# Kernel optimization log

Measured on AMD Instinct MI355X. Metric: run time of the kernel, lower is better.

## Reference

```python
import jax, jax.numpy as jnp
import numpy as np


def setup_inputs() -> dict:
    key = jax.random.key(0)
    B, C, L = 8, 32, 131072
    x = jax.random.normal(key, (B, C, L), dtype=jnp.float32)
    return {"x": x, "kernel_size": 9}


def reference(x, kernel_size):
    # x: [B, C, L]; replicate-pad last dim by (k-1)//2 on each side,
    # take sliding windows of size k, return per-window median.
    k = kernel_size
    p = (k - 1) // 2
    L = x.shape[-1]
    xp = jnp.pad(x, ((0, 0), (0, 0), (p, p)), mode="edge")  # [B, C, L+k-1]
    # Stack k shifted views -> [k, B, C, L] (loop over small fixed k only)
    win = jnp.stack([xp[..., i:i + L] for i in range(k)], axis=0)
    # k is odd, so the exact middle of the sorted window is the median
    # (matches torch.median's lower-median convention for odd k).
    return jnp.sort(win, axis=0)[k // 2]
```

## Files before the change

kernel.cpp:

```cpp
#include <hip/hip_runtime.h>


typedef float f32x4 __attribute__((ext_vector_type(4)));

#define CE(a, b) do { float _mn = fminf(a, b); (b) = fmaxf(a, b); (a) = _mn; } while (0)

__device__ __forceinline__ float median9(float p0, float p1, float p2,
                                         float p3, float p4, float p5,
                                         float p6, float p7, float p8) {
    CE(p1, p2); CE(p4, p5); CE(p7, p8);
    CE(p0, p1); CE(p3, p4); CE(p6, p7);
    CE(p1, p2); CE(p4, p5); CE(p7, p8);
    CE(p0, p3); CE(p5, p8); CE(p4, p7);
    CE(p3, p6); CE(p1, p4); CE(p2, p5);
    CE(p4, p7); CE(p4, p2); CE(p6, p4);
    CE(p4, p2);
    return p4;
}

constexpr int kL         = 131072;
constexpr int kTotal     = 8 * 32 * kL;
constexpr int kPerThread = 8;

__global__ __launch_bounds__(256)
void med9_f32_kernel(const float* __restrict__ in, float* __restrict__ out) {
    int t    = blockIdx.x * 256 + threadIdx.x;
    int base = t * kPerThread;
    int col  = base & (kL - 1);
    const float* __restrict__ rin = in + (base - col);

    float v[16];
    if (col >= 4 && col + 12 <= kL) {
        f32x4 a = *reinterpret_cast<const f32x4*>(rin + col - 4);
        f32x4 b = *reinterpret_cast<const f32x4*>(rin + col);
        f32x4 c = *reinterpret_cast<const f32x4*>(rin + col + 4);
        f32x4 d = *reinterpret_cast<const f32x4*>(rin + col + 8);
        v[0]  = a.x; v[1]  = a.y; v[2]  = a.z; v[3]  = a.w;
        v[4]  = b.x; v[5]  = b.y; v[6]  = b.z; v[7]  = b.w;
        v[8]  = c.x; v[9]  = c.y; v[10] = c.z; v[11] = c.w;
        v[12] = d.x; v[13] = d.y; v[14] = d.z; v[15] = d.w;
    } else {
#pragma unroll
        for (int j = 0; j < 16; ++j) {
            int idx = col - 4 + j;
            idx = idx < 0 ? 0 : (idx > kL - 1 ? kL - 1 : idx);
            v[j] = rin[idx];
        }
    }

    f32x4 r0, r1;
    r0.x = median9(v[0], v[1], v[2],  v[3],  v[4],  v[5],  v[6],  v[7],  v[8]);
    r0.y = median9(v[1], v[2], v[3],  v[4],  v[5],  v[6],  v[7],  v[8],  v[9]);
    r0.z = median9(v[2], v[3], v[4],  v[5],  v[6],  v[7],  v[8],  v[9],  v[10]);
    r0.w = median9(v[3], v[4], v[5],  v[6],  v[7],  v[8],  v[9],  v[10], v[11]);
    r1.x = median9(v[4], v[5], v[6],  v[7],  v[8],  v[9],  v[10], v[11], v[12]);
    r1.y = median9(v[5], v[6], v[7],  v[8],  v[9],  v[10], v[11], v[12], v[13]);
    r1.z = median9(v[6], v[7], v[8],  v[9],  v[10], v[11], v[12], v[13], v[14]);
    r1.w = median9(v[7], v[8], v[9],  v[10], v[11], v[12], v[13], v[14], v[15]);

    __builtin_nontemporal_store(r0, reinterpret_cast<f32x4*>(out + base));
    __builtin_nontemporal_store(r1, reinterpret_cast<f32x4*>(out + base + 4));
}

extern "C" void kernel_launch(void* const* d_in, const int* in_sizes, int n_in,
                              void* d_out, int out_size, void* d_ws, size_t ws_size,
                              hipStream_t stream) {
    const float* x = (const float*)d_in[0];
    float* out = (float*)d_out;

    int nthreads = kTotal / kPerThread;
    int block = 256;
    int grid = nthreads / block;
    med9_f32_kernel<<<grid, block, 0, stream>>>(x, out);
}
```

Measured before the change: 54.43 us.

## Compute 9-point median via shared 3-element sorted triples and fmed3

Replaces the per-output 19-compare-exchange median network with the classic median-of-medians decomposition. Each consecutive triple of inputs is reduced once to min, med and max using min3/max3/fmed3, and every output's median is then taken from three overlapping triples. The triples are shared across the 8 outputs each thread produces, which cuts ALU work. Nontemporal stores are also replaced by regular stores. The kernel is likely memory-bound, so the reduced arithmetic may matter little.

```diff
diff --git a/kernel.cpp b/kernel.cpp
--- a/kernel.cpp
+++ b/kernel.cpp
@@ -3,29 +3,22 @@
 
 typedef float f32x4 __attribute__((ext_vector_type(4)));
 
-#define CE(a, b) do { float _mn = fminf(a, b); (b) = fmaxf(a, b); (a) = _mn; } while (0)
-
-__device__ __forceinline__ float median9(float p0, float p1, float p2,
-                                         float p3, float p4, float p5,
-                                         float p6, float p7, float p8) {
-    CE(p1, p2); CE(p4, p5); CE(p7, p8);
-    CE(p0, p1); CE(p3, p4); CE(p6, p7);
-    CE(p1, p2); CE(p4, p5); CE(p7, p8);
-    CE(p0, p3); CE(p5, p8); CE(p4, p7);
-    CE(p3, p6); CE(p1, p4); CE(p2, p5);
-    CE(p4, p7); CE(p4, p2); CE(p6, p4);
-    CE(p4, p2);
-    return p4;
+__device__ __forceinline__ float min3f(float a, float b, float c) {
+    return fminf(fminf(a, b), c);
+}
+__device__ __forceinline__ float max3f(float a, float b, float c) {
+    return fmaxf(fmaxf(a, b), c);
+}
+__device__ __forceinline__ float med3f(float a, float b, float c) {
+    return __builtin_amdgcn_fmed3f(a, b, c);
 }
 
-constexpr int kL         = 131072;
-constexpr int kTotal     = 8 * 32 * kL;
-constexpr int kPerThread = 8;
+constexpr int kL     = 131072;
+constexpr int kTotal = 8 * 32 * kL;
 
 __global__ __launch_bounds__(256)
 void med9_f32_kernel(const float* __restrict__ in, float* __restrict__ out) {
-    int t    = blockIdx.x * 256 + threadIdx.x;
-    int base = t * kPerThread;
+    int base = (blockIdx.x * 256 + threadIdx.x) * 8;
     int col  = base & (kL - 1);
     const float* __restrict__ rin = in + (base - col);
 
@@ -48,18 +41,27 @@
         }
     }
 
-    f32x4 r0, r1;
-    r0.x = median9(v[0], v[1], v[2],  v[3],  v[4],  v[5],  v[6],  v[7],  v[8]);
-    r0.y = median9(v[1], v[2], v[3],  v[4],  v[5],  v[6],  v[7],  v[8],  v[9]);
-    r0.z = median9(v[2], v[3], v[4],  v[5],  v[6],  v[7],  v[8],  v[9],  v[10]);
-    r0.w = median9(v[3], v[4], v[5],  v[6],  v[7],  v[8],  v[9],  v[10], v[11]);
-    r1.x = median9(v[4], v[5], v[6],  v[7],  v[8],  v[9],  v[10], v[11], v[12]);
-    r1.y = median9(v[5], v[6], v[7],  v[8],  v[9],  v[10], v[11], v[12], v[13]);
-    r1.z = median9(v[6], v[7], v[8],  v[9],  v[10], v[11], v[12], v[13], v[14]);
-    r1.w = median9(v[7], v[8], v[9],  v[10], v[11], v[12], v[13], v[14], v[15]);
+    float lo[14], mi[14], hi[14];
+#pragma unroll
+    for (int j = 0; j < 14; ++j) {
+        lo[j] = min3f(v[j], v[j + 1], v[j + 2]);
+        mi[j] = med3f(v[j], v[j + 1], v[j + 2]);
+        hi[j] = max3f(v[j], v[j + 1], v[j + 2]);
+    }
 
-    __builtin_nontemporal_store(r0, reinterpret_cast<f32x4*>(out + base));
-    __builtin_nontemporal_store(r1, reinterpret_cast<f32x4*>(out + base + 4));
+    float r[8];
+#pragma unroll
+    for (int t = 0; t < 8; ++t) {
+        float P = max3f(lo[t], lo[t + 3], lo[t + 6]);
+        float Q = med3f(mi[t], mi[t + 3], mi[t + 6]);
+        float R = min3f(hi[t], hi[t + 3], hi[t + 6]);
+        r[t] = med3f(P, Q, R);
+    }
+
+    f32x4 r0 = { r[0], r[1], r[2], r[3] };
+    f32x4 r1 = { r[4], r[5], r[6], r[7] };
+    *reinterpret_cast<f32x4*>(out + base)     = r0;
+    *reinterpret_cast<f32x4*>(out + base + 4) = r1;
 }
 
 extern "C" void kernel_launch(void* const* d_in, const int* in_sizes, int n_in,
@@ -68,8 +70,6 @@
     const float* x = (const float*)d_in[0];
     float* out = (float*)d_out;
 
-    int nthreads = kTotal / kPerThread;
-    int block = 256;
-    int grid = nthreads / block;
-    med9_f32_kernel<<<grid, block, 0, stream>>>(x, out);
+    int grid = kTotal / (256 * 8);
+    med9_f32_kernel<<<grid, 256, 0, stream>>>(x, out);
 }
```

Result: faster. 44.71 us, median of 2 (-17.8%).
